# Performance work log

Hardware: AMD Instinct MI355X
Metric: run time of the kernel (lower is better)

Reference implementation:

```python
import jax, jax.numpy as jnp
import numpy as np


def setup_inputs() -> dict:
    key = jax.random.key(0)
    k1, k2, k3 = jax.random.split(key, 3)
    bsz, seqlen = 1024, 200
    vocab, d = 100000, 512
    xs = jax.random.randint(k1, (bsz, seqlen), 0, vocab, dtype=jnp.int64)
    lt_weight = jax.random.normal(k2, (vocab, d), dtype=jnp.float32)
    # freqs[i] = 1/(1+log(1+freq)) in the original -> positive weights in (0,1]
    freqs = jax.random.uniform(k3, (vocab,), dtype=jnp.float32, minval=0.05, maxval=1.0)
    return {"xs": xs, "lt_weight": lt_weight, "freqs": freqs}


def reference(xs, lt_weight, freqs):
    # embedding lookup: [bsz, len, d]
    xs_emb = lt_weight[xs]
    # vectorized replacement of the per-element python double loop:
    # x_scale[j, i] = freqs[xs[j, i]]  -> [bsz, len]
    x_scale = freqs[xs]
    # normalize by Frobenius norm of the whole [bsz, len] matrix (torch .norm())
    x_scale = x_scale / jnp.linalg.norm(x_scale)
    # weighted pooling: xs_emb^T @ x_scale -> [bsz, d]
    return jnp.einsum("bld,bl->bd", xs_emb, x_scale)
```

## Files before the change

kernel.cpp:

```cpp
#include <hip/hip_runtime.h>

#define SEQ        200
#define DIM        512
#define SSQ_BLOCKS 256

__global__ __launch_bounds__(256) void ssq_partial(const int* __restrict__ xs,
                                                   const float* __restrict__ freqs,
                                                   double* __restrict__ partials,
                                                   int n) {
    float acc = 0.f;
    for (int i = blockIdx.x * 256 + threadIdx.x; i < n; i += SSQ_BLOCKS * 256) {
        float f = freqs[xs[i]];
        acc += f * f;
    }
    double accd = (double)acc;
    for (int off = 32; off > 0; off >>= 1)
        accd += __shfl_down(accd, off, 64);
    __shared__ double s_w[4];
    if ((threadIdx.x & 63) == 0) s_w[threadIdx.x >> 6] = accd;
    __syncthreads();
    if (threadIdx.x == 0)
        partials[blockIdx.x] = s_w[0] + s_w[1] + s_w[2] + s_w[3];
}

__global__ __launch_bounds__(512) void pool_kernel(const int* __restrict__ xs,
                                                   const float* __restrict__ W,
                                                   const float* __restrict__ freqs,
                                                   const double* __restrict__ partials,
                                                   float* __restrict__ out) {
    __shared__ int    s_idx[SEQ];
    __shared__ float  s_scl[SEQ];
    __shared__ float  s_part[3][DIM];
    __shared__ double s_w[8];
    __shared__ float  s_inv;

    const int b   = blockIdx.x;
    const int tid = threadIdx.x;

    double v = (tid < SSQ_BLOCKS) ? partials[tid] : 0.0;
    for (int off = 32; off > 0; off >>= 1)
        v += __shfl_down(v, off, 64);
    if ((tid & 63) == 0) s_w[tid >> 6] = v;
    __syncthreads();
    if (tid == 0) {
        double t = 0.0;
        for (int w = 0; w < 8; ++w) t += s_w[w];
        s_inv = (float)(1.0 / sqrt(t));
    }
    __syncthreads();
    const float inv_norm = s_inv;

    for (int l = tid; l < SEQ; l += 512) {
        int idx  = xs[(size_t)b * SEQ + l];
        s_idx[l] = idx;
        s_scl[l] = freqs[idx] * inv_norm;
    }
    __syncthreads();

    const int group   = tid >> 7;
    const int lane128 = tid & 127;
    const int col4    = lane128 * 4;

    float4 acc = make_float4(0.f, 0.f, 0.f, 0.f);

    #pragma unroll 1
    for (int c = 0; c < SEQ / 4; c += 5) {
        float4 wv[5];
        float  sv[5];
        #pragma unroll
        for (int k = 0; k < 5; ++k) {
            const int l = group + 4 * (c + k);
            const int idx = s_idx[l];
            sv[k] = s_scl[l];
            wv[k] = *reinterpret_cast<const float4*>(
                W + (size_t)idx * DIM + col4);
        }
        #pragma unroll
        for (int k = 0; k < 5; ++k) {
            acc.x += sv[k] * wv[k].x;
            acc.y += sv[k] * wv[k].y;
            acc.z += sv[k] * wv[k].z;
            acc.w += sv[k] * wv[k].w;
        }
    }

    if (group > 0)
        *reinterpret_cast<float4*>(&s_part[group - 1][col4]) = acc;
    __syncthreads();
    if (group == 0) {
        for (int g = 0; g < 3; ++g) {
            const float4 p = *reinterpret_cast<const float4*>(&s_part[g][col4]);
            acc.x += p.x; acc.y += p.y; acc.z += p.z; acc.w += p.w;
        }
        *reinterpret_cast<float4*>(out + (size_t)b * DIM + col4) = acc;
    }
}

extern "C" void kernel_launch(void* const* d_in, const int* in_sizes, int n_in,
                              void* d_out, int out_size, void* d_ws, size_t ws_size,
                              hipStream_t stream) {
    const int*   xs    = (const int*)d_in[0];
    const float* W     = (const float*)d_in[1];
    const float* freqs = (const float*)d_in[2];
    float*  out      = (float*)d_out;
    double* partials = (double*)d_ws;

    const int n   = in_sizes[0];
    const int bsz = n / SEQ;

    ssq_partial<<<SSQ_BLOCKS, 256, 0, stream>>>(xs, freqs, partials, n);
    pool_kernel<<<bsz, 512, 0, stream>>>(xs, W, freqs, partials, out);
}
```

Baseline: 68.48 us.

## Fuse sum-of-squares into pool kernel and apply global norm in rescale pass

Drops the separate sum-of-squares kernel. Each pool block now computes its own row's partial sum while loading indices and frequencies, pools with unnormalized weights, and writes its per-row partial. A small rescale kernel then reduces all partials and multiplies the output by the inverse norm. This removes an extra pass over the indices and freqs gather and a barrier before pooling, at the cost of an extra read-modify-write of the output. The gather loop is also unrolled to 10 loads per iteration instead of 5 to keep more memory requests in flight.

```diff
diff --git a/kernel.cpp b/kernel.cpp
--- a/kernel.cpp
+++ b/kernel.cpp
@@ -1,61 +1,41 @@
 #include <hip/hip_runtime.h>
 
-#define SEQ        200
-#define DIM        512
-#define SSQ_BLOCKS 256
-
-__global__ __launch_bounds__(256) void ssq_partial(const int* __restrict__ xs,
-                                                   const float* __restrict__ freqs,
-                                                   double* __restrict__ partials,
-                                                   int n) {
-    float acc = 0.f;
-    for (int i = blockIdx.x * 256 + threadIdx.x; i < n; i += SSQ_BLOCKS * 256) {
-        float f = freqs[xs[i]];
-        acc += f * f;
-    }
-    double accd = (double)acc;
-    for (int off = 32; off > 0; off >>= 1)
-        accd += __shfl_down(accd, off, 64);
-    __shared__ double s_w[4];
-    if ((threadIdx.x & 63) == 0) s_w[threadIdx.x >> 6] = accd;
-    __syncthreads();
-    if (threadIdx.x == 0)
-        partials[blockIdx.x] = s_w[0] + s_w[1] + s_w[2] + s_w[3];
-}
+#define SEQ  200
+#define DIM  512
+#define BSZ_BLOCKS 1024
+#define RS_BLOCKS  256
 
 __global__ __launch_bounds__(512) void pool_kernel(const int* __restrict__ xs,
                                                    const float* __restrict__ W,
                                                    const float* __restrict__ freqs,
-                                                   const double* __restrict__ partials,
+                                                   double* __restrict__ partials,
                                                    float* __restrict__ out) {
     __shared__ int    s_idx[SEQ];
-    __shared__ float  s_scl[SEQ];
+    __shared__ float  s_f[SEQ];
     __shared__ float  s_part[3][DIM];
     __shared__ double s_w[8];
-    __shared__ float  s_inv;
 
     const int b   = blockIdx.x;
     const int tid = threadIdx.x;
 
-    double v = (tid < SSQ_BLOCKS) ? partials[tid] : 0.0;
+    float ssl = 0.f;
+    for (int l = tid; l < SEQ; l += 512) {
+        int   idx = xs[(size_t)b * SEQ + l];
+        float f   = freqs[idx];
+        s_idx[l] = idx;
+        s_f[l]   = f;
+        ssl += f * f;
+    }
+    double accd = (double)ssl;
     for (int off = 32; off > 0; off >>= 1)
-        v += __shfl_down(v, off, 64);
-    if ((tid & 63) == 0) s_w[tid >> 6] = v;
+        accd += __shfl_down(accd, off, 64);
+    if ((tid & 63) == 0) s_w[tid >> 6] = accd;
     __syncthreads();
     if (tid == 0) {
         double t = 0.0;
         for (int w = 0; w < 8; ++w) t += s_w[w];
-        s_inv = (float)(1.0 / sqrt(t));
+        partials[b] = t;
     }
-    __syncthreads();
-    const float inv_norm = s_inv;
-
-    for (int l = tid; l < SEQ; l += 512) {
-        int idx  = xs[(size_t)b * SEQ + l];
-        s_idx[l] = idx;
-        s_scl[l] = freqs[idx] * inv_norm;
-    }
-    __syncthreads();
 
     const int group   = tid >> 7;
     const int lane128 = tid & 127;
@@ -64,19 +44,19 @@
     float4 acc = make_float4(0.f, 0.f, 0.f, 0.f);
 
     #pragma unroll 1
-    for (int c = 0; c < SEQ / 4; c += 5) {
-        float4 wv[5];
-        float  sv[5];
+    for (int c = 0; c < SEQ / 4; c += 10) {
+        float4 wv[10];
+        float  sv[10];
         #pragma unroll
-        for (int k = 0; k < 5; ++k) {
-            const int l = group + 4 * (c + k);
+        for (int k = 0; k < 10; ++k) {
+            const int l   = group + 4 * (c + k);
             const int idx = s_idx[l];
-            sv[k] = s_scl[l];
+            sv[k] = s_f[l];
             wv[k] = *reinterpret_cast<const float4*>(
                 W + (size_t)idx * DIM + col4);
         }
         #pragma unroll
-        for (int k = 0; k < 5; ++k) {
+        for (int k = 0; k < 10; ++k) {
             acc.x += sv[k] * wv[k].x;
             acc.y += sv[k] * wv[k].y;
             acc.z += sv[k] * wv[k].z;
@@ -96,6 +76,38 @@
     }
 }
 
+__global__ __launch_bounds__(256) void rescale_kernel(const double* __restrict__ partials,
+                                                      float* __restrict__ out) {
+    __shared__ double s_w[4];
+    __shared__ float  s_inv;
+
+    const int tid = threadIdx.x;
+
+    double v = 0.0;
+    #pragma unroll
+    for (int k = 0; k < BSZ_BLOCKS / 256; ++k)
+        v += partials[tid + 256 * k];
+    for (int off = 32; off > 0; off >>= 1)
+        v += __shfl_down(v, off, 64);
+    if ((tid & 63) == 0) s_w[tid >> 6] = v;
+    __syncthreads();
+    if (tid == 0) {
+        double t = s_w[0] + s_w[1] + s_w[2] + s_w[3];
+        s_inv = (float)(1.0 / sqrt(t));
+    }
+    __syncthreads();
+    const float inv = s_inv;
+
+    const int base = (blockIdx.x * 256 + tid) * 2;
+    float4* o4 = reinterpret_cast<float4*>(out);
+    #pragma unroll
+    for (int k = 0; k < 2; ++k) {
+        float4 o = o4[base + k];
+        o.x *= inv; o.y *= inv; o.z *= inv; o.w *= inv;
+        o4[base + k] = o;
+    }
+}
+
 extern "C" void kernel_launch(void* const* d_in, const int* in_sizes, int n_in,
                               void* d_out, int out_size, void* d_ws, size_t ws_size,
                               hipStream_t stream) {
@@ -108,6 +120,6 @@
     const int n   = in_sizes[0];
     const int bsz = n / SEQ;
 
-    ssq_partial<<<SSQ_BLOCKS, 256, 0, stream>>>(xs, freqs, partials, n);
     pool_kernel<<<bsz, 512, 0, stream>>>(xs, W, freqs, partials, out);
+    rescale_kernel<<<RS_BLOCKS, 256, 0, stream>>>(partials, out);
 }
```

Measured after the change: 67.52 us. No clear change (-1.4%).
